# Optimization experiments

Hardware: AMD Instinct MI355X
Metric: run time of the kernel (lower is better)

Reference implementation:

```python
import jax, jax.numpy as jnp
import numpy as np

N = 50000      # nodes
E = 800000     # edges
C = 128        # dim_feat / channels
D = 256        # dim_dense
OUT = 2        # dim_out
L = 5          # num_layers - 1 GCN2Conv layers
ALPHA = 0.1    # main_param -> GCN2Conv alpha; theta=None -> beta=1.0
SLOPE = 0.01   # LeakyReLU default negative slope


def setup_inputs() -> dict:
    key = jax.random.key(0)
    ks = jax.random.split(key, 6)
    x = jax.random.normal(ks[0], (N, C), jnp.float32)
    edge_index = jax.random.randint(ks[1], (2, E), 0, N, jnp.int32)
    conv_weights = jax.random.normal(ks[2], (L, C, C), jnp.float32) * (1.0 / np.sqrt(C))
    w_dense = jax.random.normal(ks[3], (C, D), jnp.float32) * (1.0 / np.sqrt(C))
    b_dense = jnp.zeros((D,), jnp.float32)
    w_out = jax.random.normal(ks[4], (D, OUT), jnp.float32) * (1.0 / np.sqrt(D))
    b_out = jnp.zeros((OUT,), jnp.float32)
    return dict(x=x, edge_index=edge_index, conv_weights=conv_weights,
                w_dense=w_dense, b_dense=b_dense, w_out=w_out, b_out=b_out)


def _gcn_norm(edge_index, num_nodes):
    """Symmetric gcn_norm with self-loops: returns row, col, D^-1/2 * D^-1/2 edge weights."""
    loop = jnp.arange(num_nodes, dtype=edge_index.dtype)
    row = jnp.concatenate([edge_index[0], loop])  # sources
    col = jnp.concatenate([edge_index[1], loop])  # targets (aggregation index)
    ones = jnp.ones(row.shape[0], jnp.float32)
    deg = jax.ops.segment_sum(ones, col, num_segments=num_nodes)
    dinv = jnp.where(deg > 0, jax.lax.rsqrt(jnp.maximum(deg, 1e-12)), 0.0)
    return row, col, dinv[row] * dinv[col]


def reference(x, edge_index, conv_weights, w_dense, b_dense, w_out, b_out):
    num_nodes = x.shape[0]
    row, col, norm = _gcn_norm(edge_index, num_nodes)
    x0 = x
    for l in range(conv_weights.shape[0]):
        # propagate: h[i] = sum_{j->i} norm * x[j]   (gather -> scatter-add)
        h = jax.ops.segment_sum(norm[:, None] * x[row], col, num_segments=num_nodes)
        # GCN2Conv with shared_weights=True, beta=1 (theta=None): out = ((1-a)h + a*x0) @ W
        out = (1.0 - ALPHA) * h + ALPHA * x0
        x = jax.nn.leaky_relu(out @ conv_weights[l], negative_slope=SLOPE)
    x = x @ w_dense + b_dense
    return x @ w_out + b_out
```

## Files before the change

kernel.cpp:

```cpp
#include <hip/hip_runtime.h>
#include <hip/hip_fp16.h>

#define C 128
#define NOUT 2
#define ALPHA 0.1f
#define SLOPE 0.01f
#define ZP 136

typedef _Float16 half4v __attribute__((ext_vector_type(4)));
typedef float float4v __attribute__((ext_vector_type(4)));


__global__ void count_kernel(const int* __restrict__ col, int* __restrict__ cnt,
                             int* __restrict__ rank, int E) {
    int e = blockIdx.x * 256 + threadIdx.x;
    if (e < E) rank[e] = atomicAdd(&cnt[col[e]], 1);
}

__global__ __launch_bounds__(1024) void scanA_kernel(const int* __restrict__ cnt,
                                                     int* __restrict__ offs,
                                                     int* __restrict__ bsum,
                                                     float* __restrict__ dinv, int n) {
    __shared__ int wsum[16];
    int t = threadIdx.x, lane = t & 63, wv = t >> 6;
    int i = blockIdx.x * 1024 + t;
    int v = (i < n) ? cnt[i] : 0;
    if (i < n) dinv[i] = rsqrtf((float)(v + 1));
    int sc = v;
    #pragma unroll
    for (int d = 1; d < 64; d <<= 1) {
        int u = __shfl_up(sc, d);
        if (lane >= d) sc += u;
    }
    if (lane == 63) wsum[wv] = sc;
    __syncthreads();
    int woff = 0;
    #pragma unroll
    for (int j = 0; j < 16; ++j) woff += (j < wv) ? wsum[j] : 0;
    if (i < n) offs[i] = woff + sc - v;
    if (t == 0) {
        int tot = 0;
        #pragma unroll
        for (int j = 0; j < 16; ++j) tot += wsum[j];
        bsum[blockIdx.x] = tot;
    }
}

__global__ __launch_bounds__(1024) void scanB_kernel(const int* __restrict__ bsum,
                                                     int* __restrict__ bbase, int nb) {
    __shared__ int wsum[16];
    int t = threadIdx.x, lane = t & 63, wv = t >> 6;
    int v = (t < nb) ? bsum[t] : 0;
    int sc = v;
    #pragma unroll
    for (int d = 1; d < 64; d <<= 1) {
        int u = __shfl_up(sc, d);
        if (lane >= d) sc += u;
    }
    if (lane == 63) wsum[wv] = sc;
    __syncthreads();
    int woff = 0;
    #pragma unroll
    for (int j = 0; j < 16; ++j) woff += (j < wv) ? wsum[j] : 0;
    if (t < nb) bbase[t] = woff + sc - v;
}

__global__ __launch_bounds__(256) void prep_kernel(
    int* __restrict__ offs, const int* __restrict__ bbase, int n, int E,
    const float* __restrict__ x, __half* __restrict__ xh,
    const float* __restrict__ W, _Float16* __restrict__ WT, int wtot,
    const float* __restrict__ wd, _Float16* __restrict__ WDT,
    int SC, int CV, int WTB)
{
    int b = blockIdx.x;
    if (b < SC) {
        int i = b * 256 + threadIdx.x;
        if (i < n) offs[i] = offs[i] + bbase[i >> 10];
        if (i == n) offs[n] = E;
    } else if (b < SC + CV) {
        int g = (b - SC) * 256 + threadIdx.x;
        if (g >= n * 32) return;
        float4 v = ((const float4*)x)[g];
        union { __half2 h; unsigned u; } a2, b2;
        a2.h = __float22half2_rn(make_float2(v.x, v.y));
        b2.h = __float22half2_rn(make_float2(v.z, v.w));
        ((uint2*)xh)[g] = make_uint2(a2.u, b2.u);
    } else if (b < SC + CV + WTB) {
        int idx = (b - SC - CV) * 256 + threadIdx.x;
        if (idx >= wtot) return;
        int l = idx >> 14, rem = idx & 16383;
        int nrow = rem >> 7, kk = rem & 127;
        WT[idx] = (_Float16)W[(l << 14) + kk * C + nrow];
    } else {
        int idx = (b - SC - CV - WTB) * 256 + threadIdx.x;
        if (idx >= 256 * C) return;
        int nrow = idx >> 7, kk = idx & 127;
        WDT[idx] = (_Float16)wd[kk * 256 + nrow];
    }
}

__global__ void fill_kernel(const int* __restrict__ row, const int* __restrict__ col,
                            const float* __restrict__ dinv, const int* __restrict__ offs,
                            const int* __restrict__ rank, unsigned* __restrict__ csr, int E) {
    int base = blockIdx.x * 2048 + threadIdx.x;
    #pragma unroll
    for (int j = 0; j < 8; ++j) {
        int e = base + j * 256;
        if (e < E) {
            int r = row[e], c = col[e];
            union { __half h; unsigned short u; } nh;
            nh.h = __float2half_rn(dinv[r] * dinv[c]);
            csr[offs[c] + rank[e]] = ((unsigned)r << 16) | (unsigned)nh.u;
        }
    }
}

__device__ __forceinline__ void accum8(float* a, uint4 q, float w) {
    union { unsigned u; __half2 h; } c;
    float2 f;
    c.u = q.x; f = __half22float2(c.h); a[0] += w * f.x; a[1] += w * f.y;
    c.u = q.y; f = __half22float2(c.h); a[2] += w * f.x; a[3] += w * f.y;
    c.u = q.z; f = __half22float2(c.h); a[4] += w * f.x; a[5] += w * f.y;
    c.u = q.w; f = __half22float2(c.h); a[6] += w * f.x; a[7] += w * f.y;
}

__device__ __forceinline__ uint4 pack8(const float* a) {
    union { __half2 h; unsigned u; } c0, c1, c2, c3;
    c0.h = __float22half2_rn(make_float2(a[0], a[1]));
    c1.h = __float22half2_rn(make_float2(a[2], a[3]));
    c2.h = __float22half2_rn(make_float2(a[4], a[5]));
    c3.h = __float22half2_rn(make_float2(a[6], a[7]));
    return make_uint4(c0.u, c1.u, c2.u, c3.u);
}

__device__ __forceinline__ float norm_of(unsigned m) {
    union { unsigned short u; __half h; } nh;
    nh.u = (unsigned short)(m & 0xffffu);
    return __half2float(nh.h);
}

__global__ __launch_bounds__(256) void agg_kernel(
    const __half* __restrict__ xc, const __half* __restrict__ x0h,
    const int* __restrict__ offs, const unsigned* __restrict__ csr,
    const float* __restrict__ dinv, __half* __restrict__ z, int n)
{
    int node = blockIdx.x * 8 + (threadIdx.x >> 5);
    if (node >= n) return;
    int l32 = threadIdx.x & 31;
    int sub = l32 >> 4;
    int cg = l32 & 15;
    const uint4* x4 = (const uint4*)xc;
    uint4 qs = x4[(size_t)node * 16 + cg];
    uint4 q0x = ((const uint4*)x0h)[(size_t)node * 16 + cg];
    float di = dinv[node];

    float a0[8] = {}, a1[8] = {}, a2[8] = {}, a3[8] = {};
    int beg = offs[node], end = offs[node + 1];
    int k = beg + sub;
    for (; k + 14 < end; k += 16) {
        unsigned m0 = csr[k], m1 = csr[k + 2], m2 = csr[k + 4], m3 = csr[k + 6];
        unsigned m4 = csr[k + 8], m5 = csr[k + 10], m6 = csr[k + 12], m7 = csr[k + 14];
        uint4 q0 = x4[(size_t)(m0 >> 16) * 16 + cg];
        uint4 q1 = x4[(size_t)(m1 >> 16) * 16 + cg];
        uint4 q2 = x4[(size_t)(m2 >> 16) * 16 + cg];
        uint4 q3 = x4[(size_t)(m3 >> 16) * 16 + cg];
        uint4 q4 = x4[(size_t)(m4 >> 16) * 16 + cg];
        uint4 q5 = x4[(size_t)(m5 >> 16) * 16 + cg];
        uint4 q6 = x4[(size_t)(m6 >> 16) * 16 + cg];
        uint4 q7 = x4[(size_t)(m7 >> 16) * 16 + cg];
        accum8(a0, q0, norm_of(m0));
        accum8(a1, q1, norm_of(m1));
        accum8(a2, q2, norm_of(m2));
        accum8(a3, q3, norm_of(m3));
        accum8(a0, q4, norm_of(m4));
        accum8(a1, q5, norm_of(m5));
        accum8(a2, q6, norm_of(m6));
        accum8(a3, q7, norm_of(m7));
    }
    for (; k + 6 < end; k += 8) {
        unsigned m0 = csr[k], m1 = csr[k + 2], m2 = csr[k + 4], m3 = csr[k + 6];
        uint4 q0 = x4[(size_t)(m0 >> 16) * 16 + cg];
        uint4 q1 = x4[(size_t)(m1 >> 16) * 16 + cg];
        uint4 q2 = x4[(size_t)(m2 >> 16) * 16 + cg];
        uint4 q3 = x4[(size_t)(m3 >> 16) * 16 + cg];
        accum8(a0, q0, norm_of(m0));
        accum8(a1, q1, norm_of(m1));
        accum8(a2, q2, norm_of(m2));
        accum8(a3, q3, norm_of(m3));
    }
    for (; k < end; k += 2) {
        unsigned m = csr[k];
        uint4 q = x4[(size_t)(m >> 16) * 16 + cg];
        accum8(a0, q, norm_of(m));
    }
    #pragma unroll
    for (int j = 0; j < 8; ++j) a0[j] += a1[j] + a2[j] + a3[j];
    #pragma unroll
    for (int j = 0; j < 8; ++j) a0[j] += __shfl_xor(a0[j], 16);
    if (sub == 0) {
        float sw = di * di;
        accum8(a0, qs, sw);
        float xr[8] = {};
        accum8(xr, q0x, 1.f);
        float zz[8];
        #pragma unroll
        for (int j = 0; j < 8; ++j) zz[j] = (1.f - ALPHA) * a0[j] + ALPHA * xr[j];
        ((uint4*)z)[(size_t)node * 16 + cg] = pack8(zz);
    }
}

__global__ __launch_bounds__(512) void layer_mfma(
    const __half* __restrict__ zin, const _Float16* __restrict__ WT,
    __half* __restrict__ xn, int n)
{
    __shared__ _Float16 zl[64 * ZP];
    __shared__ _Float16 ol[64 * ZP];
    int i0 = blockIdx.x * 64;
    int t = threadIdx.x;
    int w = t >> 6, lane = t & 63;
    int c = lane & 15, g = lane >> 4;

    const uint4* z4 = (const uint4*)zin;
    #pragma unroll
    for (int p = t; p < 64 * 16; p += 512) {
        int r = p >> 4, c8 = p & 15;
        uint4 zv = make_uint4(0, 0, 0, 0);
        if (i0 + r < n) zv = z4[(size_t)(i0 + r) * 16 + c8];
        *(uint4*)&zl[r * ZP + c8 * 8] = zv;
    }

    half4v bf[8];
    #pragma unroll
    for (int kb = 0; kb < 8; ++kb)
        bf[kb] = *(const half4v*)&WT[(w * 16 + c) * C + kb * 16 + 4 * g];

    __syncthreads();

    #pragma unroll
    for (int m = 0; m < 4; ++m) {
        const _Float16* arow = &zl[(m * 16 + c) * ZP];
        half4v af[8];
        #pragma unroll
        for (int kb = 0; kb < 8; ++kb) af[kb] = *(const half4v*)&arow[kb * 16 + 4 * g];
        float4v acc = (float4v)0.f;
        #pragma unroll
        for (int kb = 0; kb < 8; ++kb)
            acc = __builtin_amdgcn_mfma_f32_16x16x16f16(af[kb], bf[kb], acc, 0, 0, 0);
        #pragma unroll
        for (int r = 0; r < 4; ++r) {
            float v = acc[r];
            v = v > 0.f ? v : SLOPE * v;
            ol[(m * 16 + 4 * g + r) * ZP + w * 16 + c] = (_Float16)v;
        }
    }
    __syncthreads();
    #pragma unroll
    for (int p = t; p < 64 * 16; p += 512) {
        int r = p >> 4, c8 = p & 15;
        int node = i0 + r;
        if (node < n)
            ((uint4*)xn)[(size_t)node * 16 + c8] = *(uint4*)&ol[r * ZP + c8 * 8];
    }
}

__global__ __launch_bounds__(256) void dense_mfma(
    const __half* __restrict__ xin, const _Float16* __restrict__ WDT,
    const float* __restrict__ bd, const float* __restrict__ wo,
    const float* __restrict__ bo, float* __restrict__ out, int n)
{
    __shared__ _Float16 xl[64 * ZP];
    __shared__ float pp[64][4][2];
    int i0 = blockIdx.x * 64;
    int t = threadIdx.x;
    int w = t >> 6, lane = t & 63;
    int c = lane & 15, g = lane >> 4;

    const uint4* g4 = (const uint4*)xin;
    for (int p = t; p < 64 * 16; p += 256) {
        int r = p >> 4, c8 = p & 15;
        uint4 v = make_uint4(0, 0, 0, 0);
        if (i0 + r < n) v = g4[(size_t)(i0 + r) * 16 + c8];
        *(uint4*)&xl[r * ZP + c8 * 8] = v;
    }

    half4v bf[8][4];
    #pragma unroll
    for (int kb = 0; kb < 8; ++kb)
        #pragma unroll
        for (int nt = 0; nt < 4; ++nt)
            bf[kb][nt] = *(const half4v*)&WDT[((w * 4 + nt) * 16 + c) * C + kb * 16 + 4 * g];
    float bdv[4], wo0[4], wo1[4];
    #pragma unroll
    for (int nt = 0; nt < 4; ++nt) {
        int coln = (w * 4 + nt) * 16 + c;
        bdv[nt] = bd[coln];
        wo0[nt] = wo[coln * 2 + 0];
        wo1[nt] = wo[coln * 2 + 1];
    }

    __syncthreads();

    #pragma unroll
    for (int m = 0; m < 4; ++m) {
        const _Float16* arow = &xl[(m * 16 + c) * ZP];
        half4v af[8];
        #pragma unroll
        for (int kb = 0; kb < 8; ++kb) af[kb] = *(const half4v*)&arow[kb * 16 + 4 * g];
        float4v acc[4];
        #pragma unroll
        for (int nt = 0; nt < 4; ++nt) acc[nt] = (float4v)0.f;
        #pragma unroll
        for (int kb = 0; kb < 8; ++kb) {
            #pragma unroll
            for (int nt = 0; nt < 4; ++nt)
                acc[nt] = __builtin_amdgcn_mfma_f32_16x16x16f16(af[kb], bf[kb][nt], acc[nt], 0, 0, 0);
        }
        float p0[4] = {0.f, 0.f, 0.f, 0.f}, p1[4] = {0.f, 0.f, 0.f, 0.f};
        #pragma unroll
        for (int nt = 0; nt < 4; ++nt) {
            #pragma unroll
            for (int r = 0; r < 4; ++r) {
                float hv = acc[nt][r] + bdv[nt];
                p0[r] += hv * wo0[nt];
                p1[r] += hv * wo1[nt];
            }
        }
        #pragma unroll
        for (int ms = 1; ms <= 8; ms <<= 1) {
            #pragma unroll
            for (int r = 0; r < 4; ++r) {
                p0[r] += __shfl_xor(p0[r], ms);
                p1[r] += __shfl_xor(p1[r], ms);
            }
        }
        if (c == 0) {
            #pragma unroll
            for (int r = 0; r < 4; ++r) {
                pp[m * 16 + 4 * g + r][w][0] = p0[r];
                pp[m * 16 + 4 * g + r][w][1] = p1[r];
            }
        }
    }
    __syncthreads();
    if (t < 128) {
        int r = t >> 1, o = t & 1;
        int node = i0 + r;
        if (node < n) {
            float s = pp[r][0][o] + pp[r][1][o] + pp[r][2][o] + pp[r][3][o];
            out[(size_t)node * NOUT + o] = s + bo[o];
        }
    }
}

extern "C" void kernel_launch(void* const* d_in, const int* in_sizes, int n_in,
                              void* d_out, int out_size, void* d_ws, size_t ws_size,
                              hipStream_t stream) {
    const float* x0    = (const float*)d_in[0];
    const int*   ei    = (const int*)d_in[1];
    const float* convW = (const float*)d_in[2];
    const float* wd    = (const float*)d_in[3];
    const float* bd    = (const float*)d_in[4];
    const float* wo    = (const float*)d_in[5];
    const float* bo    = (const float*)d_in[6];
    float* out = (float*)d_out;

    int N = in_sizes[0] / C;
    int E = in_sizes[1] / 2;
    int L = in_sizes[2] / (C * C);
    const int* row = ei;
    const int* col = ei + E;
    int NB = (N + 1023) / 1024;

    char* p = (char*)d_ws;
    auto alloc = [&](size_t bytes) {
        char* r = p;
        p += (bytes + 255) & ~(size_t)255;
        return r;
    };
    int*      cnt    = (int*)alloc((size_t)N * 4);
    int*      offs   = (int*)alloc((size_t)(N + 1) * 4);
    int*      rank   = (int*)alloc((size_t)E * 4);
    int*      bsum   = (int*)alloc((size_t)NB * 4);
    int*      bbase  = (int*)alloc((size_t)NB * 4);
    unsigned* csr    = (unsigned*)alloc((size_t)E * 4);
    float*    dinv   = (float*)alloc((size_t)N * 4);
    __half*   x0h    = (__half*)alloc((size_t)N * C * 2);
    __half*   bufA   = (__half*)alloc((size_t)N * C * 2);
    __half*   zbuf   = (__half*)alloc((size_t)N * C * 2);
    _Float16* WT     = (_Float16*)alloc((size_t)L * C * C * 2);
    _Float16* WDT    = (_Float16*)alloc((size_t)256 * C * 2);

    hipMemsetAsync(cnt, 0, (size_t)N * 4, stream);
    count_kernel<<<(E + 255) / 256, 256, 0, stream>>>(col, cnt, rank, E);
    scanA_kernel<<<NB, 1024, 0, stream>>>(cnt, offs, bsum, dinv, N);
    scanB_kernel<<<1, 1024, 0, stream>>>(bsum, bbase, NB);
    int wtot = L * C * C;
    int SC  = (N + 256) / 256;
    int CV  = (N * 32 + 255) / 256;
    int WTB = (wtot + 255) / 256;
    int WDB = (256 * C + 255) / 256;
    prep_kernel<<<SC + CV + WTB + WDB, 256, 0, stream>>>(
        offs, bbase, N, E, x0, x0h, convW, WT, wtot, wd, WDT, SC, CV, WTB);
    fill_kernel<<<(E + 2047) / 2048, 256, 0, stream>>>(row, col, dinv, offs, rank, csr, E);

    const __half* xc = x0h;
    for (int l = 0; l < L; ++l) {
        agg_kernel<<<(N + 7) / 8, 256, 0, stream>>>(xc, x0h, offs, csr, dinv, zbuf, N);
        layer_mfma<<<(N + 63) / 64, 512, 0, stream>>>(zbuf, WT + (size_t)l * C * C,
                                                      bufA, N);
        xc = bufA;
    }
    dense_mfma<<<(N + 63) / 64, 256, 0, stream>>>(xc, WDT, bd, wo, bo, out, N);
}
```

Before: 366.0 us.

## Fuse neighbor aggregation with per-layer MFMA matmul into one kernel

Merges the gather/aggregate kernel and the per-layer weight matmul into a single kernel. Each block of 256 threads aggregates 32 nodes into shared memory, then multiplies them by the layer weights with MFMA, two N-tiles per wave. This removes the fp16 z intermediate round trip through global memory and one launch per layer. Buffers now ping-pong because the kernel reads xc and writes the next layer's input. The cost is more weight-fragment loads per block (32 rows instead of 64), serialized aggregation of four nodes per half-wave, and higher register pressure.

```diff
diff --git a/kernel.cpp b/kernel.cpp
--- a/kernel.cpp
+++ b/kernel.cpp
@@ -139,123 +139,123 @@
     return __half2float(nh.h);
 }
 
-__global__ __launch_bounds__(256) void agg_kernel(
+__global__ __launch_bounds__(256) void layer_fused(
     const __half* __restrict__ xc, const __half* __restrict__ x0h,
     const int* __restrict__ offs, const unsigned* __restrict__ csr,
-    const float* __restrict__ dinv, __half* __restrict__ z, int n)
+    const float* __restrict__ dinv, const _Float16* __restrict__ WT,
+    __half* __restrict__ xn, int n)
 {
-    int node = blockIdx.x * 8 + (threadIdx.x >> 5);
-    if (node >= n) return;
-    int l32 = threadIdx.x & 31;
+    __shared__ _Float16 zl[32 * ZP];
+    __shared__ _Float16 ol[32 * ZP];
+    int i0 = blockIdx.x * 32;
+    int t = threadIdx.x;
+    int hw = t >> 5;
+    int l32 = t & 31;
     int sub = l32 >> 4;
     int cg = l32 & 15;
     const uint4* x4 = (const uint4*)xc;
-    uint4 qs = x4[(size_t)node * 16 + cg];
-    uint4 q0x = ((const uint4*)x0h)[(size_t)node * 16 + cg];
-    float di = dinv[node];
-
-    float a0[8] = {}, a1[8] = {}, a2[8] = {}, a3[8] = {};
-    int beg = offs[node], end = offs[node + 1];
-    int k = beg + sub;
-    for (; k + 14 < end; k += 16) {
-        unsigned m0 = csr[k], m1 = csr[k + 2], m2 = csr[k + 4], m3 = csr[k + 6];
-        unsigned m4 = csr[k + 8], m5 = csr[k + 10], m6 = csr[k + 12], m7 = csr[k + 14];
-        uint4 q0 = x4[(size_t)(m0 >> 16) * 16 + cg];
-        uint4 q1 = x4[(size_t)(m1 >> 16) * 16 + cg];
-        uint4 q2 = x4[(size_t)(m2 >> 16) * 16 + cg];
-        uint4 q3 = x4[(size_t)(m3 >> 16) * 16 + cg];
-        uint4 q4 = x4[(size_t)(m4 >> 16) * 16 + cg];
-        uint4 q5 = x4[(size_t)(m5 >> 16) * 16 + cg];
-        uint4 q6 = x4[(size_t)(m6 >> 16) * 16 + cg];
-        uint4 q7 = x4[(size_t)(m7 >> 16) * 16 + cg];
-        accum8(a0, q0, norm_of(m0));
-        accum8(a1, q1, norm_of(m1));
-        accum8(a2, q2, norm_of(m2));
-        accum8(a3, q3, norm_of(m3));
-        accum8(a0, q4, norm_of(m4));
-        accum8(a1, q5, norm_of(m5));
-        accum8(a2, q6, norm_of(m6));
-        accum8(a3, q7, norm_of(m7));
-    }
-    for (; k + 6 < end; k += 8) {
-        unsigned m0 = csr[k], m1 = csr[k + 2], m2 = csr[k + 4], m3 = csr[k + 6];
-        uint4 q0 = x4[(size_t)(m0 >> 16) * 16 + cg];
-        uint4 q1 = x4[(size_t)(m1 >> 16) * 16 + cg];
-        uint4 q2 = x4[(size_t)(m2 >> 16) * 16 + cg];
-        uint4 q3 = x4[(size_t)(m3 >> 16) * 16 + cg];
-        accum8(a0, q0, norm_of(m0));
-        accum8(a1, q1, norm_of(m1));
-        accum8(a2, q2, norm_of(m2));
-        accum8(a3, q3, norm_of(m3));
-    }
-    for (; k < end; k += 2) {
-        unsigned m = csr[k];
-        uint4 q = x4[(size_t)(m >> 16) * 16 + cg];
-        accum8(a0, q, norm_of(m));
-    }
-    #pragma unroll
-    for (int j = 0; j < 8; ++j) a0[j] += a1[j] + a2[j] + a3[j];
-    #pragma unroll
-    for (int j = 0; j < 8; ++j) a0[j] += __shfl_xor(a0[j], 16);
-    if (sub == 0) {
-        float sw = di * di;
-        accum8(a0, qs, sw);
-        float xr[8] = {};
-        accum8(xr, q0x, 1.f);
-        float zz[8];
-        #pragma unroll
-        for (int j = 0; j < 8; ++j) zz[j] = (1.f - ALPHA) * a0[j] + ALPHA * xr[j];
-        ((uint4*)z)[(size_t)node * 16 + cg] = pack8(zz);
-    }
-}
-
-__global__ __launch_bounds__(512) void layer_mfma(
-    const __half* __restrict__ zin, const _Float16* __restrict__ WT,
-    __half* __restrict__ xn, int n)
-{
-    __shared__ _Float16 zl[64 * ZP];
-    __shared__ _Float16 ol[64 * ZP];
-    int i0 = blockIdx.x * 64;
-    int t = threadIdx.x;
+
+    #pragma unroll 1
+    for (int j = 0; j < 4; ++j) {
+        int r = hw * 4 + j;
+        int node = i0 + r;
+        if (node < n) {
+            uint4 qs = x4[(size_t)node * 16 + cg];
+            uint4 q0x = ((const uint4*)x0h)[(size_t)node * 16 + cg];
+            float di = dinv[node];
+
+            float a0[8] = {}, a1[8] = {}, a2[8] = {}, a3[8] = {};
+            int beg = offs[node], end = offs[node + 1];
+            int k = beg + sub;
+            for (; k + 14 < end; k += 16) {
+                unsigned m0 = csr[k], m1 = csr[k + 2], m2 = csr[k + 4], m3 = csr[k + 6];
+                unsigned m4 = csr[k + 8], m5 = csr[k + 10], m6 = csr[k + 12], m7 = csr[k + 14];
+                uint4 q0 = x4[(size_t)(m0 >> 16) * 16 + cg];
+                uint4 q1 = x4[(size_t)(m1 >> 16) * 16 + cg];
+                uint4 q2 = x4[(size_t)(m2 >> 16) * 16 + cg];
+                uint4 q3 = x4[(size_t)(m3 >> 16) * 16 + cg];
+                uint4 q4 = x4[(size_t)(m4 >> 16) * 16 + cg];
+                uint4 q5 = x4[(size_t)(m5 >> 16) * 16 + cg];
+                uint4 q6 = x4[(size_t)(m6 >> 16) * 16 + cg];
+                uint4 q7 = x4[(size_t)(m7 >> 16) * 16 + cg];
+                accum8(a0, q0, norm_of(m0));
+                accum8(a1, q1, norm_of(m1));
+                accum8(a2, q2, norm_of(m2));
+                accum8(a3, q3, norm_of(m3));
+                accum8(a0, q4, norm_of(m4));
+                accum8(a1, q5, norm_of(m5));
+                accum8(a2, q6, norm_of(m6));
+                accum8(a3, q7, norm_of(m7));
+            }
+            for (; k + 6 < end; k += 8) {
+                unsigned m0 = csr[k], m1 = csr[k + 2], m2 = csr[k + 4], m3 = csr[k + 6];
+                uint4 q0 = x4[(size_t)(m0 >> 16) * 16 + cg];
+                uint4 q1 = x4[(size_t)(m1 >> 16) * 16 + cg];
+                uint4 q2 = x4[(size_t)(m2 >> 16) * 16 + cg];
+                uint4 q3 = x4[(size_t)(m3 >> 16) * 16 + cg];
+                accum8(a0, q0, norm_of(m0));
+                accum8(a1, q1, norm_of(m1));
+                accum8(a2, q2, norm_of(m2));
+                accum8(a3, q3, norm_of(m3));
+            }
+            for (; k < end; k += 2) {
+                unsigned m = csr[k];
+                uint4 q = x4[(size_t)(m >> 16) * 16 + cg];
+                accum8(a0, q, norm_of(m));
+            }
+            #pragma unroll
+            for (int q = 0; q < 8; ++q) a0[q] += a1[q] + a2[q] + a3[q];
+            #pragma unroll
+            for (int q = 0; q < 8; ++q) a0[q] += __shfl_xor(a0[q], 16);
+            if (sub == 0) {
+                float sw = di * di;
+                accum8(a0, qs, sw);
+                float xr[8] = {};
+                accum8(xr, q0x, 1.f);
+                float zz[8];
+                #pragma unroll
+                for (int q = 0; q < 8; ++q) zz[q] = (1.f - ALPHA) * a0[q] + ALPHA * xr[q];
+                *(uint4*)&zl[r * ZP + cg * 8] = pack8(zz);
+            }
+        } else if (sub == 0) {
+            *(uint4*)&zl[r * ZP + cg * 8] = make_uint4(0, 0, 0, 0);
+        }
+    }
+
     int w = t >> 6, lane = t & 63;
     int c = lane & 15, g = lane >> 4;
-
-    const uint4* z4 = (const uint4*)zin;
-    #pragma unroll
-    for (int p = t; p < 64 * 16; p += 512) {
-        int r = p >> 4, c8 = p & 15;
-        uint4 zv = make_uint4(0, 0, 0, 0);
-        if (i0 + r < n) zv = z4[(size_t)(i0 + r) * 16 + c8];
-        *(uint4*)&zl[r * ZP + c8 * 8] = zv;
-    }
-
-    half4v bf[8];
+    half4v bf[8][2];
     #pragma unroll
     for (int kb = 0; kb < 8; ++kb)
-        bf[kb] = *(const half4v*)&WT[(w * 16 + c) * C + kb * 16 + 4 * g];
-
-    __syncthreads();
-
-    #pragma unroll
-    for (int m = 0; m < 4; ++m) {
+        #pragma unroll
+        for (int nt = 0; nt < 2; ++nt)
+            bf[kb][nt] = *(const half4v*)&WT[((w * 2 + nt) * 16 + c) * C + kb * 16 + 4 * g];
+
+    __syncthreads();
+
+    #pragma unroll
+    for (int m = 0; m < 2; ++m) {
         const _Float16* arow = &zl[(m * 16 + c) * ZP];
         half4v af[8];
         #pragma unroll
         for (int kb = 0; kb < 8; ++kb) af[kb] = *(const half4v*)&arow[kb * 16 + 4 * g];
-        float4v acc = (float4v)0.f;
-        #pragma unroll
-        for (int kb = 0; kb < 8; ++kb)
-            acc = __builtin_amdgcn_mfma_f32_16x16x16f16(af[kb], bf[kb], acc, 0, 0, 0);
+        float4v acc0 = (float4v)0.f, acc1 = (float4v)0.f;
+        #pragma unroll
+        for (int kb = 0; kb < 8; ++kb) {
+            acc0 = __builtin_amdgcn_mfma_f32_16x16x16f16(af[kb], bf[kb][0], acc0, 0, 0, 0);
+            acc1 = __builtin_amdgcn_mfma_f32_16x16x16f16(af[kb], bf[kb][1], acc1, 0, 0, 0);
+        }
         #pragma unroll
         for (int r = 0; r < 4; ++r) {
-            float v = acc[r];
-            v = v > 0.f ? v : SLOPE * v;
-            ol[(m * 16 + 4 * g + r) * ZP + w * 16 + c] = (_Float16)v;
-        }
-    }
-    __syncthreads();
-    #pragma unroll
-    for (int p = t; p < 64 * 16; p += 512) {
+            float v0 = acc0[r]; v0 = v0 > 0.f ? v0 : SLOPE * v0;
+            float v1 = acc1[r]; v1 = v1 > 0.f ? v1 : SLOPE * v1;
+            ol[(m * 16 + 4 * g + r) * ZP + (w * 2 + 0) * 16 + c] = (_Float16)v0;
+            ol[(m * 16 + 4 * g + r) * ZP + (w * 2 + 1) * 16 + c] = (_Float16)v1;
+        }
+    }
+    __syncthreads();
+    #pragma unroll
+    for (int p = t; p < 32 * 16; p += 256) {
         int r = p >> 4, c8 = p & 15;
         int node = i0 + r;
         if (node < n)
@@ -386,7 +386,7 @@
     float*    dinv   = (float*)alloc((size_t)N * 4);
     __half*   x0h    = (__half*)alloc((size_t)N * C * 2);
     __half*   bufA   = (__half*)alloc((size_t)N * C * 2);
-    __half*   zbuf   = (__half*)alloc((size_t)N * C * 2);
+    __half*   bufB   = (__half*)alloc((size_t)N * C * 2);
     _Float16* WT     = (_Float16*)alloc((size_t)L * C * C * 2);
     _Float16* WDT    = (_Float16*)alloc((size_t)256 * C * 2);
 
@@ -405,10 +405,10 @@
 
     const __half* xc = x0h;
     for (int l = 0; l < L; ++l) {
-        agg_kernel<<<(N + 7) / 8, 256, 0, stream>>>(xc, x0h, offs, csr, dinv, zbuf, N);
-        layer_mfma<<<(N + 63) / 64, 512, 0, stream>>>(zbuf, WT + (size_t)l * C * C,
-                                                      bufA, N);
-        xc = bufA;
+        __half* nxt = (l & 1) ? bufB : bufA;
+        layer_fused<<<(N + 31) / 32, 256, 0, stream>>>(
+            xc, x0h, offs, csr, dinv, WT + (size_t)l * C * C, nxt, N);
+        xc = nxt;
     }
     dense_mfma<<<(N + 63) / 64, 256, 0, stream>>>(xc, WDT, bd, wo, bo, out, N);
 }
```

Measured after the change: 392.3 us. 1.07x slower.
